# Kernel optimization log

Hardware: AMD Instinct MI355X
Metric: run time of the kernel (lower is better)

The kernel has to match this reference:

```python
import jax, jax.numpy as jnp
import numpy as np

B, C, H, W = 2, 4, 32, 256   # batch, num_classes (class 0 = background), range-image H x W
N = H * W                    # candidate points per (batch, class)
RADIUS = 3.0
KM_ITERS = 1
COORD_SCALE = 60.0           # spread lidar x/y so radius-3 NMS is non-trivial


def setup_inputs() -> dict:
    key = jax.random.key(0)
    k1, k2 = jax.random.split(key)
    segmented_channels = jax.random.normal(k1, (B, C, H, W), dtype=jnp.float32)
    lidar = jax.random.normal(k2, (B, 2, H, W), dtype=jnp.float32) * COORD_SCALE
    return {"segmented_channels": segmented_channels, "lidar": lidar}


def _radius_nms(points, mask, radius):
    # Greedy radius NMS in index order: keep point i iff no earlier kept point
    # lies within `radius`. Masked-out points are never kept (keep init = mask).
    n = points.shape[0]
    idx = jnp.arange(n)
    r2 = radius * radius

    def step(keep, i):
        d2 = jnp.sum((points - points[i]) ** 2, axis=-1)       # [N]
        suppress = keep & (d2 < r2) & (idx > i) & keep[i]
        return keep & ~suppress, None

    keep, _ = jax.lax.scan(step, mask, idx)
    return keep


def _kmeans(points, mask, keep, iters):
    # Centers initialized at the NMS-kept points (same index space as points).
    # Each valid class point is assigned to nearest valid center; centers move
    # to the mean of their assigned points.
    n = points.shape[0]
    centers = points
    w = mask.astype(points.dtype)
    BIG = jnp.asarray(1e30, points.dtype)
    for _ in range(iters):
        d2 = jnp.sum((points[:, None, :] - centers[None, :, :]) ** 2, axis=-1)  # [N,N]
        d2 = jnp.where(keep[None, :], d2, BIG)
        assign = jnp.argmin(d2, axis=1)                         # [N]
        sums = jax.ops.segment_sum(points * w[:, None], assign, num_segments=n)
        cnt = jax.ops.segment_sum(w, assign, num_segments=n)
        upd = sums / jnp.maximum(cnt, 1.0)[:, None]
        centers = jnp.where((keep & (cnt > 0))[:, None], upd, centers)
    return centers * keep[:, None].astype(points.dtype)


def reference(segmented_channels, lidar):
    ind = jnp.argmax(segmented_channels, axis=1)                # [B,H,W] class id per cell
    pts = jnp.stack([lidar[:, 0], lidar[:, 1]], axis=-1).reshape(B, N, 2)
    # boolean class masks for foreground classes 1..C-1
    cls_mask = jnp.stack([ind == c for c in range(1, C)], axis=1).reshape(B, C - 1, N)
    pts_all = jnp.broadcast_to(pts[:, None], (B, C - 1, N, 2)).reshape(B * (C - 1), N, 2)
    mask_all = cls_mask.reshape(B * (C - 1), N)

    def per_bc(args):
        p, m = args
        keep = _radius_nms(p, m, RADIUS)
        centers = _kmeans(p, m, keep, KM_ITERS)
        return centers, keep

    centers, keep = jax.lax.map(per_bc, (pts_all, mask_all))
    # centers: padded [B, C-1, N, 2]; keep marks which rows are real detections
    return centers.reshape(B, C - 1, N, 2), keep.reshape(B, C - 1, N)
```

## Files before the change

kernel.cpp:

```cpp
#include <hip/hip_runtime.h>

#define NPTS 8192
#define BCLS 4
#define NP   6
#define R2   9.0f
#define RAD  3.0f
#define GRD  64
#define NCELL (GRD*GRD)
#define PCAP 4096

#define ST_U 0
#define ST_A 1
#define ST_D 2

__global__ __launch_bounds__(1024) void k_fused(
    const float* __restrict__ seg, const float* __restrict__ lidar,
    float* __restrict__ sumx, float* __restrict__ sumy, float* __restrict__ cntw,
    float* __restrict__ out)
{
    const int p = blockIdx.x;
    const int b = p / 3, cls = p % 3 + 1;
    const int tid = threadIdx.x, lane = tid & 63, wv = tid >> 6;
    const int base = p * NPTS;

    __shared__ float2 sp[NPTS];
    __shared__ unsigned short cidx[NPTS];
    __shared__ unsigned short sortid[NPTS];
    __shared__ unsigned int cellpack[NCELL];
    __shared__ unsigned char st[NPTS];
    __shared__ unsigned short plist[2][PCAP];
    __shared__ int pcnt[2];
    __shared__ unsigned long long ballots[128];
    __shared__ unsigned int base128[128];
    __shared__ unsigned int wtot[16];
    __shared__ float redbuf[4][16];
    __shared__ float sbminx, sbminy, scell;
    __shared__ int sM;

    float* ok = out + (size_t)2 * NP * NPTS + base;

    for (int k = tid; k < NPTS; k += 1024) {
        st[k] = ST_U;
        sumx[base + k] = 0.f; sumy[base + k] = 0.f; cntw[base + k] = 0.f;
        ok[k] = 0.f;
    }
    {
        float2* oc = (float2*)(out + (size_t)2 * base);
        for (int k = tid; k < NPTS; k += 1024) oc[k] = make_float2(0.f, 0.f);
    }
    for (int k = tid; k < NCELL; k += 1024) cellpack[k] = 0u;
    if (tid == 0) { pcnt[0] = 0; pcnt[1] = 0; }

    const float* segb = seg + (size_t)b * BCLS * NPTS;
    const float* lx = lidar + (size_t)b * 2 * NPTS;
    const float* ly = lx + NPTS;
    for (int c0 = 0; c0 < 8; ++c0) {
        int n = c0 * 1024 + tid;
        float bv = segb[n];
        int bc = 0;
        #pragma unroll
        for (int c2 = 1; c2 < BCLS; ++c2) {
            float v = segb[c2 * NPTS + n];
            if (v > bv) { bv = v; bc = c2; }
        }
        unsigned long long bal = __ballot(bc == cls);
        if (lane == 0) ballots[c0 * 16 + wv] = bal;
    }
    __syncthreads();
    if (tid == 0) {
        unsigned int acc = 0;
        for (int q = 0; q < 128; ++q) { base128[q] = acc; acc += __popcll(ballots[q]); }
        sM = (int)acc;
    }
    __syncthreads();
    const int M = sM;
    for (int c0 = 0; c0 < 8; ++c0) {
        unsigned long long bal = ballots[c0 * 16 + wv];
        if ((bal >> lane) & 1ull) {
            int n = c0 * 1024 + tid;
            int pos = (int)base128[c0 * 16 + wv] + __popcll(bal & ((1ull << lane) - 1ull));
            sp[pos] = make_float2(lx[n], ly[n]);
            cidx[pos] = (unsigned short)n;
        }
    }
    __syncthreads();

    {
        float mnx = 3e38f, mxx = -3e38f, mny = 3e38f, mxy = -3e38f;
        for (int i = tid; i < M; i += 1024) {
            float2 q = sp[i];
            mnx = fminf(mnx, q.x); mxx = fmaxf(mxx, q.x);
            mny = fminf(mny, q.y); mxy = fmaxf(mxy, q.y);
        }
        for (int d = 32; d; d >>= 1) {
            mnx = fminf(mnx, __shfl_xor(mnx, d, 64));
            mxx = fmaxf(mxx, __shfl_xor(mxx, d, 64));
            mny = fminf(mny, __shfl_xor(mny, d, 64));
            mxy = fmaxf(mxy, __shfl_xor(mxy, d, 64));
        }
        if (lane == 0) { redbuf[0][wv] = mnx; redbuf[1][wv] = mxx;
                         redbuf[2][wv] = mny; redbuf[3][wv] = mxy; }
    }
    __syncthreads();
    if (tid == 0) {
        float a = redbuf[0][0], b2 = redbuf[1][0], c = redbuf[2][0], d = redbuf[3][0];
        for (int q = 1; q < 16; ++q) {
            a = fminf(a, redbuf[0][q]); b2 = fmaxf(b2, redbuf[1][q]);
            c = fminf(c, redbuf[2][q]); d = fmaxf(d, redbuf[3][q]);
        }
        sbminx = a; sbminy = c;
        scell = fmaxf(2.0f * RAD, fmaxf(b2 - a, d - c) / 63.0f);
    }
    __syncthreads();
    const float bminx = sbminx, bminy = sbminy, inv = 1.0f / scell;

    for (int i = tid; i < M; i += 1024) {
        float2 q = sp[i];
        int ix = min(GRD - 1, max(0, (int)((q.x - bminx) * inv)));
        int iy = min(GRD - 1, max(0, (int)((q.y - bminy) * inv)));
        atomicAdd(&cellpack[iy * GRD + ix], 1u);
    }
    __syncthreads();
    {
        unsigned int c4[4], t4 = 0;
        #pragma unroll
        for (int q = 0; q < 4; ++q) { c4[q] = cellpack[tid * 4 + q]; t4 += c4[q]; }
        unsigned int v = t4;
        for (int d = 1; d < 64; d <<= 1) {
            unsigned int u = __shfl_up(v, d, 64);
            if (lane >= d) v += u;
        }
        if (lane == 63) wtot[wv] = v;
        __syncthreads();
        if (tid == 0) {
            unsigned int acc = 0;
            for (int q = 0; q < 16; ++q) { unsigned int t = wtot[q]; wtot[q] = acc; acc += t; }
        }
        __syncthreads();
        unsigned int excl = wtot[wv] + v - t4;
        #pragma unroll
        for (int q = 0; q < 4; ++q) {
            cellpack[tid * 4 + q] = excl << 16;
            excl += c4[q];
        }
    }
    __syncthreads();
    for (int i = tid; i < M; i += 1024) {
        float2 q = sp[i];
        int ix = min(GRD - 1, max(0, (int)((q.x - bminx) * inv)));
        int iy = min(GRD - 1, max(0, (int)((q.y - bminy) * inv)));
        unsigned int old = atomicAdd(&cellpack[iy * GRD + ix], 1u);
        sortid[(old >> 16) + (old & 0xffffu)] = (unsigned short)i;
    }
    __syncthreads();

    #define SCAN_WIN(I, ME, DEAD, UNDEC)                                          \
    {                                                                             \
        int cx0 = max(0, (int)((ME.x - RAD - bminx) * inv));                      \
        int cx1 = min(GRD - 1, (int)((ME.x + RAD - bminx) * inv));                \
        int cy0 = max(0, (int)((ME.y - RAD - bminy) * inv));                      \
        int cy1 = min(GRD - 1, (int)((ME.y + RAD - bminy) * inv));                \
        DEAD = false; UNDEC = false;                                              \
        for (int cy = cy0; cy <= cy1; ++cy)                                       \
            for (int cx = cx0; cx <= cx1; ++cx) {                                 \
                unsigned int w = cellpack[cy * GRD + cx];                         \
                unsigned int e0 = w >> 16, e1 = e0 + (w & 0xffffu);               \
                for (unsigned int e = e0; e < e1; ++e) {                          \
                    int j = sortid[e];                                            \
                    float2 q = sp[j];                                             \
                    unsigned char sv = st[j];                                     \
                    float dx = __fsub_rn(ME.x, q.x), dy = __fsub_rn(ME.y, q.y);   \
                    float d2 = __fadd_rn(__fmul_rn(dx, dx), __fmul_rn(dy, dy));   \
                    bool in = (d2 < R2) & (j < I);                                \
                    DEAD  |= in & (sv == ST_A);                                   \
                    UNDEC |= in & (sv == ST_U);                                   \
                }                                                                 \
            }                                                                     \
    }

    for (int i = tid; i < M; i += 1024) {
        float2 me = sp[i];
        bool dead, undec;
        SCAN_WIN(i, me, dead, undec);
        if (dead) st[i] = ST_D;
        else if (!undec) st[i] = ST_A;
        else {
            int pos = atomicAdd(&pcnt[0], 1);
            if (pos < PCAP) plist[0][pos] = (unsigned short)i;
        }
    }
    __syncthreads();
    int cur = 0;
    for (int round = 0; round < NPTS; ++round) {
        int pc = pcnt[cur];
        if (pc == 0) break;
        if (pc > PCAP) {
            for (;;) {
                bool any = false;
                __syncthreads();
                for (int i = tid; i < M; i += 1024) {
                    if (st[i] != ST_U) continue;
                    float2 me = sp[i];
                    bool dead, undec;
                    SCAN_WIN(i, me, dead, undec);
                    if (dead) st[i] = ST_D;
                    else if (!undec) st[i] = ST_A;
                    else any = true;
                }
                if (__syncthreads_count(any) == 0) break;
            }
            break;
        }
        if (tid == 0) pcnt[cur ^ 1] = 0;
        __syncthreads();
        for (int idx = tid; idx < pc; idx += 1024) {
            int i = plist[cur][idx];
            float2 me = sp[i];
            bool dead, undec;
            SCAN_WIN(i, me, dead, undec);
            if (dead) st[i] = ST_D;
            else if (!undec) st[i] = ST_A;
            else {
                int pos = atomicAdd(&pcnt[cur ^ 1], 1);
                if (pos < PCAP) plist[cur ^ 1][pos] = (unsigned short)i;
            }
        }
        __syncthreads();
        cur ^= 1;
    }

    for (int i = tid; i < M; i += 1024) {
        float2 me = sp[i];
        int bj;
        if (st[i] == ST_A) {
            bj = i;
        } else {
            int cx0 = max(0, (int)((me.x - RAD - bminx) * inv));
            int cx1 = min(GRD - 1, (int)((me.x + RAD - bminx) * inv));
            int cy0 = max(0, (int)((me.y - RAD - bminy) * inv));
            int cy1 = min(GRD - 1, (int)((me.y + RAD - bminy) * inv));
            float bd = 3e38f;
            bj = -1;
            for (int cy = cy0; cy <= cy1; ++cy)
                for (int cx = cx0; cx <= cx1; ++cx) {
                    unsigned int w = cellpack[cy * GRD + cx];
                    unsigned int e0 = w >> 16, e1 = e0 + (w & 0xffffu);
                    for (unsigned int e = e0; e < e1; ++e) {
                        int j = sortid[e];
                        float2 q = sp[j];
                        unsigned char sv = st[j];
                        float dx = __fsub_rn(me.x, q.x), dy = __fsub_rn(me.y, q.y);
                        float d2 = __fadd_rn(__fmul_rn(dx, dx), __fmul_rn(dy, dy));
                        bool better = (sv == ST_A) &
                                      ((d2 < bd) | ((d2 == bd) & (j < bj)));
                        bd = better ? d2 : bd;
                        bj = better ? j : bj;
                    }
                }
            if (bj < 0) continue;
        }
        atomicAdd(&sumx[base + bj], me.x);
        atomicAdd(&sumy[base + bj], me.y);
        atomicAdd(&cntw[base + bj], 1.0f);
    }
    __syncthreads();

    for (int i = tid; i < M; i += 1024) {
        if (st[i] != ST_A) continue;
        int n = cidx[i];
        float c = cntw[base + i];
        out[2 * (base + n)]     = sumx[base + i] / c;
        out[2 * (base + n) + 1] = sumy[base + i] / c;
        ok[n] = 1.0f;
    }
}

extern "C" void kernel_launch(void* const* d_in, const int* in_sizes, int n_in,
                              void* d_out, int out_size, void* d_ws, size_t ws_size,
                              hipStream_t stream) {
    const float* seg   = (const float*)d_in[0];
    const float* lidar = (const float*)d_in[1];
    float* out = (float*)d_out;

    const size_t A = (size_t)NP * NPTS;
    float* sumx = (float*)d_ws;
    float* sumy = sumx + A;
    float* cntw = sumy + A;

    k_fused<<<NP, 1024, 0, stream>>>(seg, lidar, sumx, sumy, cntw, out);
}
```

Before: 117.8 us.

## Accumulate k-means sums in LDS by kept-rank, row-span scans, wave-aggregated queue

Per-center k-means sums move from global atomics to shared-memory accumulators indexed by the center's rank among kept points, falling back to global memory only when there are more than LDSK kept points. This removes the workspace zeroing and the global atomic traffic in the common case. Neighbour scans now walk each grid row as one contiguous sortid range, relying on the cell being at least the radius so only two rows are needed. Points are processed in grid-sorted order for locality, pending-list appends are aggregated per wave, and the ballot prefix sum runs as a wave scan instead of a single-thread loop. In exchange the pending-list capacity is halved, so the slower full-rescan fallback triggers sooner, and an extra ballot/rank pass is added.

Result: faster. 109.5 us (-7.0%).

```diff
diff --git a/kernel.cpp b/kernel.cpp
--- a/kernel.cpp
+++ b/kernel.cpp
@@ -7,7 +7,8 @@
 #define RAD  3.0f
 #define GRD  64
 #define NCELL (GRD*GRD)
-#define PCAP 4096
+#define PCAP 2048
+#define LDSK 2048
 
 #define ST_U 0
 #define ST_A 1
@@ -29,26 +30,24 @@
     __shared__ unsigned int cellpack[NCELL];
     __shared__ unsigned char st[NPTS];
     __shared__ unsigned short plist[2][PCAP];
+    __shared__ float ksx[LDSK], ksy[LDSK], kcn[LDSK];
     __shared__ int pcnt[2];
     __shared__ unsigned long long ballots[128];
     __shared__ unsigned int base128[128];
     __shared__ unsigned int wtot[16];
     __shared__ float redbuf[4][16];
     __shared__ float sbminx, sbminy, scell;
-    __shared__ int sM;
+    __shared__ int sM, sK;
 
     float* ok = out + (size_t)2 * NP * NPTS + base;
 
-    for (int k = tid; k < NPTS; k += 1024) {
-        st[k] = ST_U;
-        sumx[base + k] = 0.f; sumy[base + k] = 0.f; cntw[base + k] = 0.f;
-        ok[k] = 0.f;
-    }
+    for (int k = tid; k < NPTS; k += 1024) { st[k] = ST_U; ok[k] = 0.f; }
     {
         float2* oc = (float2*)(out + (size_t)2 * base);
         for (int k = tid; k < NPTS; k += 1024) oc[k] = make_float2(0.f, 0.f);
     }
     for (int k = tid; k < NCELL; k += 1024) cellpack[k] = 0u;
+    for (int k = tid; k < LDSK; k += 1024) { ksx[k] = 0.f; ksy[k] = 0.f; kcn[k] = 0.f; }
     if (tid == 0) { pcnt[0] = 0; pcnt[1] = 0; }
 
     const float* segb = seg + (size_t)b * BCLS * NPTS;
@@ -67,10 +66,17 @@
         if (lane == 0) ballots[c0 * 16 + wv] = bal;
     }
     __syncthreads();
-    if (tid == 0) {
-        unsigned int acc = 0;
-        for (int q = 0; q < 128; ++q) { base128[q] = acc; acc += __popcll(ballots[q]); }
-        sM = (int)acc;
+    if (wv == 0) {
+        unsigned int p0 = (unsigned int)__popcll(ballots[2 * lane]);
+        unsigned int p1 = (unsigned int)__popcll(ballots[2 * lane + 1]);
+        unsigned int s = p0 + p1, v = s;
+        for (int d = 1; d < 64; d <<= 1) {
+            unsigned int u = __shfl_up(v, d, 64);
+            if (lane >= d) v += u;
+        }
+        base128[2 * lane] = v - s;
+        base128[2 * lane + 1] = v - p1;
+        if (lane == 63) sM = (int)v;
     }
     __syncthreads();
     const int M = sM;
@@ -139,10 +145,7 @@
         __syncthreads();
         unsigned int excl = wtot[wv] + v - t4;
         #pragma unroll
-        for (int q = 0; q < 4; ++q) {
-            cellpack[tid * 4 + q] = excl << 16;
-            excl += c4[q];
-        }
+        for (int q = 0; q < 4; ++q) { cellpack[tid * 4 + q] = excl << 16; excl += c4[q]; }
     }
     __syncthreads();
     for (int i = tid; i < M; i += 1024) {
@@ -154,44 +157,57 @@
     }
     __syncthreads();
 
-    #define SCAN_WIN(I, ME, DEAD, UNDEC)                                          \
+    #define ROW_FLAGS(CY, CX0, CX1, I, ME, DEAD, UNDEC)                           \
+    {                                                                             \
+        unsigned int wa = cellpack[(CY) * GRD + (CX0)];                           \
+        unsigned int wb = cellpack[(CY) * GRD + (CX1)];                           \
+        unsigned int e0 = wa >> 16, e1 = (wb >> 16) + (wb & 0xffffu);             \
+        for (unsigned int e = e0; e < e1; ++e) {                                  \
+            int j = sortid[e];                                                    \
+            float2 q = sp[j];                                                     \
+            unsigned char sv = st[j];                                             \
+            float dx = __fsub_rn(ME.x, q.x), dy = __fsub_rn(ME.y, q.y);           \
+            float d2 = __fadd_rn(__fmul_rn(dx, dx), __fmul_rn(dy, dy));           \
+            bool in = (d2 < R2) & (j < (I));                                      \
+            DEAD  |= in & (sv == ST_A);                                           \
+            UNDEC |= in & (sv == ST_U);                                           \
+        }                                                                         \
+    }
+    #define SCAN_FLAGS(I, ME, DEAD, UNDEC)                                        \
     {                                                                             \
         int cx0 = max(0, (int)((ME.x - RAD - bminx) * inv));                      \
         int cx1 = min(GRD - 1, (int)((ME.x + RAD - bminx) * inv));                \
         int cy0 = max(0, (int)((ME.y - RAD - bminy) * inv));                      \
         int cy1 = min(GRD - 1, (int)((ME.y + RAD - bminy) * inv));                \
         DEAD = false; UNDEC = false;                                              \
-        for (int cy = cy0; cy <= cy1; ++cy)                                       \
-            for (int cx = cx0; cx <= cx1; ++cx) {                                 \
-                unsigned int w = cellpack[cy * GRD + cx];                         \
-                unsigned int e0 = w >> 16, e1 = e0 + (w & 0xffffu);               \
-                for (unsigned int e = e0; e < e1; ++e) {                          \
-                    int j = sortid[e];                                            \
-                    float2 q = sp[j];                                             \
-                    unsigned char sv = st[j];                                     \
-                    float dx = __fsub_rn(ME.x, q.x), dy = __fsub_rn(ME.y, q.y);   \
-                    float d2 = __fadd_rn(__fmul_rn(dx, dx), __fmul_rn(dy, dy));   \
-                    bool in = (d2 < R2) & (j < I);                                \
-                    DEAD  |= in & (sv == ST_A);                                   \
-                    UNDEC |= in & (sv == ST_U);                                   \
-                }                                                                 \
-            }                                                                     \
-    }
-
-    for (int i = tid; i < M; i += 1024) {
+        ROW_FLAGS(cy0, cx0, cx1, I, ME, DEAD, UNDEC);                             \
+        if (cy1 > cy0) ROW_FLAGS(cy1, cx0, cx1, I, ME, DEAD, UNDEC);              \
+    }
+
+    for (int g = tid; g < M; g += 1024) {
+        int i = sortid[g];
         float2 me = sp[i];
         bool dead, undec;
-        SCAN_WIN(i, me, dead, undec);
+        SCAN_FLAGS(i, me, dead, undec);
         if (dead) st[i] = ST_D;
         else if (!undec) st[i] = ST_A;
-        else {
-            int pos = atomicAdd(&pcnt[0], 1);
+        bool pendf = !dead && undec;
+        unsigned long long act = __ballot(true);
+        unsigned long long bal = __ballot(pendf);
+        int leader = __builtin_ctzll(act);
+        int cnt = __popcll(bal);
+        int wbase = 0;
+        if (lane == leader && cnt) wbase = atomicAdd(&pcnt[0], cnt);
+        wbase = __shfl(wbase, leader, 64);
+        if (pendf) {
+            int pos = wbase + __popcll(bal & ((1ull << lane) - 1ull));
             if (pos < PCAP) plist[0][pos] = (unsigned short)i;
         }
     }
-    __syncthreads();
+
     int cur = 0;
     for (int round = 0; round < NPTS; ++round) {
+        __syncthreads();
         int pc = pcnt[cur];
         if (pc == 0) break;
         if (pc > PCAP) {
@@ -202,7 +218,7 @@
                     if (st[i] != ST_U) continue;
                     float2 me = sp[i];
                     bool dead, undec;
-                    SCAN_WIN(i, me, dead, undec);
+                    SCAN_FLAGS(i, me, dead, undec);
                     if (dead) st[i] = ST_D;
                     else if (!undec) st[i] = ST_A;
                     else any = true;
@@ -217,19 +233,72 @@
             int i = plist[cur][idx];
             float2 me = sp[i];
             bool dead, undec;
-            SCAN_WIN(i, me, dead, undec);
+            SCAN_FLAGS(i, me, dead, undec);
             if (dead) st[i] = ST_D;
             else if (!undec) st[i] = ST_A;
-            else {
-                int pos = atomicAdd(&pcnt[cur ^ 1], 1);
+            bool pendf = !dead && undec;
+            unsigned long long act = __ballot(true);
+            unsigned long long bal = __ballot(pendf);
+            int leader = __builtin_ctzll(act);
+            int cnt = __popcll(bal);
+            int wbase = 0;
+            if (lane == leader && cnt) wbase = atomicAdd(&pcnt[cur ^ 1], cnt);
+            wbase = __shfl(wbase, leader, 64);
+            if (pendf) {
+                int pos = wbase + __popcll(bal & ((1ull << lane) - 1ull));
                 if (pos < PCAP) plist[cur ^ 1][pos] = (unsigned short)i;
             }
         }
-        __syncthreads();
         cur ^= 1;
     }
-
-    for (int i = tid; i < M; i += 1024) {
+    __syncthreads();
+
+    for (int k = 0; k < 8; ++k) {
+        int i = (k << 10) + tid;
+        unsigned long long bal = __ballot(st[i] == ST_A);
+        if (lane == 0) ballots[(k << 4) + wv] = bal;
+    }
+    __syncthreads();
+    if (wv == 0) {
+        unsigned int p0 = (unsigned int)__popcll(ballots[2 * lane]);
+        unsigned int p1 = (unsigned int)__popcll(ballots[2 * lane + 1]);
+        unsigned int s = p0 + p1, v = s;
+        for (int d = 1; d < 64; d <<= 1) {
+            unsigned int u = __shfl_up(v, d, 64);
+            if (lane >= d) v += u;
+        }
+        base128[2 * lane] = v - s;
+        base128[2 * lane + 1] = v - p1;
+        if (lane == 63) sK = (int)v;
+    }
+    __syncthreads();
+    #define KRANK(J) ((int)base128[(J) >> 6] +                                    \
+                      __popcll(ballots[(J) >> 6] & ((1ull << ((J) & 63)) - 1ull)))
+    if (sK > LDSK) {
+        for (int k = tid; k < NPTS; k += 1024) {
+            sumx[base + k] = 0.f; sumy[base + k] = 0.f; cntw[base + k] = 0.f;
+        }
+        __syncthreads();
+    }
+
+    #define ROW_ARGMIN(CY, CX0, CX1, ME, BD, BJ)                                  \
+    {                                                                             \
+        unsigned int wa = cellpack[(CY) * GRD + (CX0)];                           \
+        unsigned int wb = cellpack[(CY) * GRD + (CX1)];                           \
+        unsigned int e0 = wa >> 16, e1 = (wb >> 16) + (wb & 0xffffu);             \
+        for (unsigned int e = e0; e < e1; ++e) {                                  \
+            int j = sortid[e];                                                    \
+            float2 q = sp[j];                                                     \
+            unsigned char sv = st[j];                                             \
+            float dx = __fsub_rn(ME.x, q.x), dy = __fsub_rn(ME.y, q.y);           \
+            float d2 = __fadd_rn(__fmul_rn(dx, dx), __fmul_rn(dy, dy));           \
+            bool better = (sv == ST_A) & ((d2 < BD) | ((d2 == BD) & (j < BJ)));   \
+            BD = better ? d2 : BD;                                                \
+            BJ = better ? j : BJ;                                                 \
+        }                                                                         \
+    }
+    for (int g = tid; g < M; g += 1024) {
+        int i = sortid[g];
         float2 me = sp[i];
         int bj;
         if (st[i] == ST_A) {
@@ -241,36 +310,32 @@
             int cy1 = min(GRD - 1, (int)((me.y + RAD - bminy) * inv));
             float bd = 3e38f;
             bj = -1;
-            for (int cy = cy0; cy <= cy1; ++cy)
-                for (int cx = cx0; cx <= cx1; ++cx) {
-                    unsigned int w = cellpack[cy * GRD + cx];
-                    unsigned int e0 = w >> 16, e1 = e0 + (w & 0xffffu);
-                    for (unsigned int e = e0; e < e1; ++e) {
-                        int j = sortid[e];
-                        float2 q = sp[j];
-                        unsigned char sv = st[j];
-                        float dx = __fsub_rn(me.x, q.x), dy = __fsub_rn(me.y, q.y);
-                        float d2 = __fadd_rn(__fmul_rn(dx, dx), __fmul_rn(dy, dy));
-                        bool better = (sv == ST_A) &
-                                      ((d2 < bd) | ((d2 == bd) & (j < bj)));
-                        bd = better ? d2 : bd;
-                        bj = better ? j : bj;
-                    }
-                }
+            ROW_ARGMIN(cy0, cx0, cx1, me, bd, bj);
+            if (cy1 > cy0) ROW_ARGMIN(cy1, cx0, cx1, me, bd, bj);
             if (bj < 0) continue;
         }
-        atomicAdd(&sumx[base + bj], me.x);
-        atomicAdd(&sumy[base + bj], me.y);
-        atomicAdd(&cntw[base + bj], 1.0f);
+        int r = KRANK(bj);
+        if (r < LDSK) {
+            atomicAdd(&ksx[r], me.x);
+            atomicAdd(&ksy[r], me.y);
+            atomicAdd(&kcn[r], 1.0f);
+        } else {
+            atomicAdd(&sumx[base + bj], me.x);
+            atomicAdd(&sumy[base + bj], me.y);
+            atomicAdd(&cntw[base + bj], 1.0f);
+        }
     }
     __syncthreads();
 
     for (int i = tid; i < M; i += 1024) {
         if (st[i] != ST_A) continue;
         int n = cidx[i];
-        float c = cntw[base + i];
-        out[2 * (base + n)]     = sumx[base + i] / c;
-        out[2 * (base + n) + 1] = sumy[base + i] / c;
+        int r = KRANK(i);
+        float sx, sy, c;
+        if (r < LDSK) { sx = ksx[r]; sy = ksy[r]; c = kcn[r]; }
+        else { sx = sumx[base + i]; sy = sumy[base + i]; c = cntw[base + i]; }
+        out[2 * (base + n)]     = sx / c;
+        out[2 * (base + n) + 1] = sy / c;
         ok[n] = 1.0f;
     }
 }
```
